# Kernel tuning notes

Hardware: AMD Instinct MI355X
Metric: run time of the kernel (lower is better)

Reference implementation:

```python
import jax, jax.numpy as jnp
import numpy as np

U, SI, TI = 100000, 50000, 40000
D = 64
B = 8192
NNZ_S, NNZ_T = 3_200_000, 2_560_000
P_DROP = 0.2


def setup_inputs() -> dict:
    key = jax.random.key(0)
    ks = iter(jax.random.split(key, 32))
    nxt = lambda: next(ks)
    emb = lambda n: (jax.random.normal(nxt(), (n, D), jnp.float32) * 0.1)
    keep = lambda n: jax.random.bernoulli(nxt(), 1.0 - P_DROP, (n,)).astype(jnp.float32) / (1.0 - P_DROP)
    inp = {}
    inp['user'] = jax.random.randint(nxt(), (B,), 0, U, jnp.int32)
    inp['source_pos_item'] = jax.random.randint(nxt(), (B,), 0, SI, jnp.int32)
    inp['source_neg_item'] = jax.random.randint(nxt(), (B,), 0, SI, jnp.int32)
    inp['target_pos_item'] = jax.random.randint(nxt(), (B,), 0, TI, jnp.int32)
    inp['target_neg_item'] = jax.random.randint(nxt(), (B,), 0, TI, jnp.int32)
    inp['mask_s'] = jax.random.bernoulli(nxt(), 0.5, (B,))
    inp['mask_t'] = jax.random.bernoulli(nxt(), 0.5, (B,))
    inp['su_int'] = emb(U); inp['si_int'] = emb(SI)
    inp['tu_int'] = emb(U); inp['ti_int'] = emb(TI)
    inp['su_pop'] = emb(U); inp['si_pop'] = emb(SI)
    inp['tu_pop'] = emb(U); inp['ti_pop'] = emb(TI)
    Ns, Nt = U + SI, U + TI
    inp['s_rows'] = jax.random.randint(nxt(), (NNZ_S,), 0, Ns, jnp.int32)
    inp['s_cols'] = jax.random.randint(nxt(), (NNZ_S,), 0, Ns, jnp.int32)
    inp['s_vals'] = jax.random.uniform(nxt(), (NNZ_S,), jnp.float32, 0.0, 0.02)
    inp['t_rows'] = jax.random.randint(nxt(), (NNZ_T,), 0, Nt, jnp.int32)
    inp['t_cols'] = jax.random.randint(nxt(), (NNZ_T,), 0, Nt, jnp.int32)
    inp['t_vals'] = jax.random.uniform(nxt(), (NNZ_T,), jnp.float32, 0.0, 0.02)
    inp['drop_s_int'] = keep(NNZ_S); inp['drop_t_int'] = keep(NNZ_T)
    inp['drop_s_pop'] = keep(NNZ_S); inp['drop_t_pop'] = keep(NNZ_T)
    return inp


def _lightgcn(emb, rows, cols, vals, n_users):
    # 1-layer LightGCN: out = mean([e0, A @ e0]) ; A given as COO (rows, cols, vals)
    agg = jax.ops.segment_sum(vals[:, None] * emb[cols], rows, num_segments=emb.shape[0])
    out = 0.5 * (emb + agg)
    return out[:n_users], out[n_users:]


def _bpr(p, n):
    return -jnp.mean(jax.nn.log_sigmoid(p - n))


def _mask_bpr(p, n, m):
    return -jnp.mean(m.astype(p.dtype) * jax.nn.log_sigmoid(p - n))


def _masked_l1(a, b, idx):
    # L1Loss(mean) over rows selected by unique(idx); membership mask avoids jnp.unique
    m = jnp.zeros((a.shape[0],), bool).at[idx].set(True)
    cnt = jnp.maximum(m.sum(), 1).astype(a.dtype)
    return jnp.sum(jnp.abs(a - b) * m[:, None]) / (cnt * a.shape[1])


def reference(user, source_pos_item, source_neg_item, target_pos_item, target_neg_item,
              mask_s, mask_t,
              su_int, si_int, tu_int, ti_int, su_pop, si_pop, tu_pop, ti_pop,
              s_rows, s_cols, s_vals, t_rows, t_cols, t_vals,
              drop_s_int, drop_t_int, drop_s_pop, drop_t_pop):
    # int factor
    us_i, is_i = _lightgcn(jnp.concatenate([su_int, si_int]), s_rows, s_cols, s_vals * drop_s_int, U)
    ut_i, it_i = _lightgcn(jnp.concatenate([tu_int, ti_int]), t_rows, t_cols, t_vals * drop_t_int, U)
    # pop factor
    us_p, is_p = _lightgcn(jnp.concatenate([su_pop, si_pop]), s_rows, s_cols, s_vals * drop_s_pop, U)
    ut_p, it_p = _lightgcn(jnp.concatenate([tu_pop, ti_pop]), t_rows, t_cols, t_vals * drop_t_pop, U)

    dot = lambda ue, ie, u, i: jnp.sum(ue[u] * ie[i], axis=1)
    sp_i = dot(us_i, is_i, user, source_pos_item); sn_i = dot(us_i, is_i, user, source_neg_item)
    sp_p = dot(us_p, is_p, user, source_pos_item); sn_p = dot(us_p, is_p, user, source_neg_item)
    tp_i = dot(ut_i, it_i, user, target_pos_item); tn_i = dot(ut_i, it_i, user, target_neg_item)
    tp_p = dot(ut_p, it_p, user, target_pos_item); tn_p = dot(ut_p, it_p, user, target_neg_item)

    loss_int_s = _mask_bpr(sp_i, sn_i, mask_s)
    loss_pop_s = _mask_bpr(sn_p, sp_p, mask_s) + _mask_bpr(sp_p, sn_p, ~mask_s)
    loss_int_t = _mask_bpr(tp_i, tn_i, mask_t)
    loss_pop_t = _mask_bpr(tn_p, tp_p, mask_t) + _mask_bpr(tp_p, tn_p, ~mask_t)
    loss_total_s = _bpr(sp_i + sp_p, sn_i + sn_p)
    loss_total_t = _bpr(tp_i + tp_p, tn_i + tn_p)

    item_all_s = jnp.concatenate([source_pos_item, source_neg_item])
    item_all_t = jnp.concatenate([target_pos_item, target_neg_item])
    dis_loss = (_masked_l1(su_int, su_pop, user) + _masked_l1(si_int, si_pop, item_all_s)
                + _masked_l1(tu_int, tu_pop, user) + _masked_l1(ti_int, ti_pop, item_all_t))

    loss = (loss_total_s + loss_total_t
            + 0.1 * (loss_int_s + loss_int_t)
            + 0.1 * (loss_pop_s + loss_pop_t)
            - 0.01 * dis_loss)
    return loss
```

## Files before the change

### kernel.cpp

```cpp
#include <hip/hip_runtime.h>
#include <math.h>

constexpr int U_N = 100000;
constexpr int SI_N = 50000;
constexpr int TI_N = 40000;
constexpr int D = 64;
constexpr int B = 8192;
constexpr int NS = U_N + SI_N;
constexpr int NT = U_N + TI_N;
constexpr int SLOTS = 3 * B;
constexpr int CAP = 64;
constexpr int OVCAP = 4096;
constexpr int NROWS_ALL = U_N + SI_N + TI_N;

__device__ __forceinline__ float wave_sum(float x) {
#pragma unroll
  for (int m = 32; m; m >>= 1) x += __shfl_xor(x, m, 64);
  return x;
}

__device__ __forceinline__ float softplus_f(float z) {
  return fmaxf(z, 0.f) + log1pf(expf(-fabsf(z)));
}

__global__ __launch_bounds__(256) void k_init(
    const int* __restrict__ user, const int* __restrict__ spos, const int* __restrict__ sneg,
    const int* __restrict__ tpos, const int* __restrict__ tneg,
    int* __restrict__ map_s, int* __restrict__ map_t,
    const unsigned char* __restrict__ m, int* __restrict__ det) {
  if (blockIdx.x < 96) {
    int t = blockIdx.x * blockDim.x + threadIdx.x;
    if (t < B) {
      int u = user[t];
      map_s[u] = t;
      map_t[u] = t;
    } else if (t < 2 * B) {
      int b = t - B;
      map_s[U_N + spos[b]] = t;
      map_t[U_N + tpos[b]] = t;
    } else {
      int b = t - 2 * B;
      map_s[U_N + sneg[b]] = t;
      map_t[U_N + tneg[b]] = t;
    }
    return;
  }
  int t = threadIdx.x;
  int cb = 0, cc = 0;
  for (int i = t; i < B; i += 256) {
    unsigned char v = m[i];
    if ((i & 3) && v) cb++;
    if (v > 1) cc++;
  }
#pragma unroll
  for (int off = 32; off; off >>= 1) {
    cb += __shfl_xor(cb, off, 64);
    cc += __shfl_xor(cc, off, 64);
  }
  __shared__ int sb[4], sc[4];
  if ((t & 63) == 0) { sb[t >> 6] = cb; sc[t >> 6] = cc; }
  __syncthreads();
  if (t == 0) {
    det[0] = sb[0] + sb[1] + sb[2] + sb[3];
    det[1] = sc[0] + sc[1] + sc[2] + sc[3];
  }
}

__global__ __launch_bounds__(256) void k_compact2(
    const int* __restrict__ s_rows, const int* __restrict__ t_rows,
    const int* __restrict__ map_s, const int* __restrict__ map_t,
    int* __restrict__ cnt_s, int* __restrict__ cnt_t,
    int* __restrict__ bucket_s, int* __restrict__ bucket_t,
    int* __restrict__ ovcnt_s, int* __restrict__ ovcnt_t,
    int* __restrict__ ov_s, int* __restrict__ ov_t, int nnz_s, int nnz_t) {
  int e = blockIdx.x * 256 + threadIdx.x;
  const int* rows;
  const int* map;
  int* cnt;
  int* bucket;
  int* ovcnt;
  int* ov;
  if (e < nnz_s) {
    rows = s_rows; map = map_s; cnt = cnt_s; bucket = bucket_s; ovcnt = ovcnt_s; ov = ov_s;
  } else {
    e -= nnz_s;
    if (e >= nnz_t) return;
    rows = t_rows; map = map_t; cnt = cnt_t; bucket = bucket_t; ovcnt = ovcnt_t; ov = ov_t;
  }
  int slot = map[rows[e]];
  if (slot < 0) return;
  int pos = atomicAdd(&cnt[slot], 1);
  if (pos < CAP) {
    bucket[slot * CAP + pos] = e;
  } else {
    int o = atomicAdd(ovcnt, 1);
    if (o < OVCAP) { ov[2 * o] = slot; ov[2 * o + 1] = e; }
  }
}

__device__ __forceinline__ void accum_slot(
    int s, int lane,
    const int* __restrict__ cols, const float* __restrict__ vals,
    const float* __restrict__ di, const float* __restrict__ dp,
    const int* __restrict__ cnt, const int* __restrict__ bucket,
    const int* __restrict__ ovcnt, const int* __restrict__ ov,
    const float* __restrict__ eu_i, const float* __restrict__ ei_i,
    const float* __restrict__ eu_p, const float* __restrict__ ei_p,
    float* __restrict__ aggA, float* __restrict__ aggB) {
  int m = min(cnt[s], CAP);
  int g = lane >> 4, sub = lane & 15;
  int c = 0;
  float wi = 0.f, wp = 0.f;
  if (lane < m) {
    int e = bucket[s * CAP + lane];
    c = cols[e];
    float v = vals[e];
    wi = v * di[e];
    wp = v * dp[e];
  }
  float aIx = 0, aIy = 0, aIz = 0, aIw = 0;
  float aPx = 0, aPy = 0, aPz = 0, aPw = 0;
  for (int k = 0; k < m; k += 16) {
    int i0 = k + g, i1 = k + 4 + g, i2 = k + 8 + g, i3 = k + 12 + g;
    int c0 = __shfl(c, i0, 64), c1 = __shfl(c, i1, 64);
    int c2 = __shfl(c, i2, 64), c3 = __shfl(c, i3, 64);
    float wi0 = __shfl(wi, i0, 64), wi1 = __shfl(wi, i1, 64);
    float wi2 = __shfl(wi, i2, 64), wi3 = __shfl(wi, i3, 64);
    float wp0 = __shfl(wp, i0, 64), wp1 = __shfl(wp, i1, 64);
    float wp2 = __shfl(wp, i2, 64), wp3 = __shfl(wp, i3, 64);
    const float* bi0 = (c0 < U_N) ? (eu_i + (size_t)c0 * D) : (ei_i + (size_t)(c0 - U_N) * D);
    const float* bi1 = (c1 < U_N) ? (eu_i + (size_t)c1 * D) : (ei_i + (size_t)(c1 - U_N) * D);
    const float* bi2 = (c2 < U_N) ? (eu_i + (size_t)c2 * D) : (ei_i + (size_t)(c2 - U_N) * D);
    const float* bi3 = (c3 < U_N) ? (eu_i + (size_t)c3 * D) : (ei_i + (size_t)(c3 - U_N) * D);
    const float* bp0 = (c0 < U_N) ? (eu_p + (size_t)c0 * D) : (ei_p + (size_t)(c0 - U_N) * D);
    const float* bp1 = (c1 < U_N) ? (eu_p + (size_t)c1 * D) : (ei_p + (size_t)(c1 - U_N) * D);
    const float* bp2 = (c2 < U_N) ? (eu_p + (size_t)c2 * D) : (ei_p + (size_t)(c2 - U_N) * D);
    const float* bp3 = (c3 < U_N) ? (eu_p + (size_t)c3 * D) : (ei_p + (size_t)(c3 - U_N) * D);
    float4 vI0 = *(const float4*)(bi0 + 4 * sub);
    float4 vI1 = *(const float4*)(bi1 + 4 * sub);
    float4 vI2 = *(const float4*)(bi2 + 4 * sub);
    float4 vI3 = *(const float4*)(bi3 + 4 * sub);
    float4 vP0 = *(const float4*)(bp0 + 4 * sub);
    float4 vP1 = *(const float4*)(bp1 + 4 * sub);
    float4 vP2 = *(const float4*)(bp2 + 4 * sub);
    float4 vP3 = *(const float4*)(bp3 + 4 * sub);
    aIx = fmaf(wi0, vI0.x, aIx); aIy = fmaf(wi0, vI0.y, aIy);
    aIz = fmaf(wi0, vI0.z, aIz); aIw = fmaf(wi0, vI0.w, aIw);
    aIx = fmaf(wi1, vI1.x, aIx); aIy = fmaf(wi1, vI1.y, aIy);
    aIz = fmaf(wi1, vI1.z, aIz); aIw = fmaf(wi1, vI1.w, aIw);
    aIx = fmaf(wi2, vI2.x, aIx); aIy = fmaf(wi2, vI2.y, aIy);
    aIz = fmaf(wi2, vI2.z, aIz); aIw = fmaf(wi2, vI2.w, aIw);
    aIx = fmaf(wi3, vI3.x, aIx); aIy = fmaf(wi3, vI3.y, aIy);
    aIz = fmaf(wi3, vI3.z, aIz); aIw = fmaf(wi3, vI3.w, aIw);
    aPx = fmaf(wp0, vP0.x, aPx); aPy = fmaf(wp0, vP0.y, aPy);
    aPz = fmaf(wp0, vP0.z, aPz); aPw = fmaf(wp0, vP0.w, aPw);
    aPx = fmaf(wp1, vP1.x, aPx); aPy = fmaf(wp1, vP1.y, aPy);
    aPz = fmaf(wp1, vP1.z, aPz); aPw = fmaf(wp1, vP1.w, aPw);
    aPx = fmaf(wp2, vP2.x, aPx); aPy = fmaf(wp2, vP2.y, aPy);
    aPz = fmaf(wp2, vP2.z, aPz); aPw = fmaf(wp2, vP2.w, aPw);
    aPx = fmaf(wp3, vP3.x, aPx); aPy = fmaf(wp3, vP3.y, aPy);
    aPz = fmaf(wp3, vP3.z, aPz); aPw = fmaf(wp3, vP3.w, aPw);
  }
#define XRED(x) x += __shfl_xor(x, 16, 64); x += __shfl_xor(x, 32, 64);
  XRED(aIx) XRED(aIy) XRED(aIz) XRED(aIw)
  XRED(aPx) XRED(aPy) XRED(aPz) XRED(aPw)
#undef XRED
  int nov = min(*ovcnt, OVCAP);
  for (int i = 0; i < nov; ++i) {
    if (ov[2 * i] == s) {
      int e = ov[2 * i + 1];
      int cc = cols[e];
      float v = vals[e];
      float wwi = v * di[e], wwp = v * dp[e];
      const float* bi = (cc < U_N) ? (eu_i + (size_t)cc * D) : (ei_i + (size_t)(cc - U_N) * D);
      const float* bp = (cc < U_N) ? (eu_p + (size_t)cc * D) : (ei_p + (size_t)(cc - U_N) * D);
      if (lane < 16) {
        float4 vI = *(const float4*)(bi + 4 * sub);
        float4 vP = *(const float4*)(bp + 4 * sub);
        aIx = fmaf(wwi, vI.x, aIx); aIy = fmaf(wwi, vI.y, aIy);
        aIz = fmaf(wwi, vI.z, aIz); aIw = fmaf(wwi, vI.w, aIw);
        aPx = fmaf(wwp, vP.x, aPx); aPy = fmaf(wwp, vP.y, aPy);
        aPz = fmaf(wwp, vP.z, aPz); aPw = fmaf(wwp, vP.w, aPw);
      }
    }
  }
  if (lane < 16) {
    *(float4*)(aggA + (size_t)s * D + 4 * sub) = make_float4(aIx, aIy, aIz, aIw);
    *(float4*)(aggB + (size_t)s * D + 4 * sub) = make_float4(aPx, aPy, aPz, aPw);
  }
}

__global__ __launch_bounds__(256) void k_accum_pair(
    const int* __restrict__ s_cols, const float* __restrict__ s_vals,
    const float* __restrict__ dsi, const float* __restrict__ dsp,
    const int* __restrict__ t_cols, const float* __restrict__ t_vals,
    const float* __restrict__ dti, const float* __restrict__ dtp,
    const int* __restrict__ cnt_s, const int* __restrict__ bucket_s,
    const int* __restrict__ ovcnt_s, const int* __restrict__ ov_s,
    const int* __restrict__ cnt_t, const int* __restrict__ bucket_t,
    const int* __restrict__ ovcnt_t, const int* __restrict__ ov_t,
    const float* __restrict__ su_i, const float* __restrict__ si_i,
    const float* __restrict__ su_p, const float* __restrict__ si_p,
    const float* __restrict__ tu_i, const float* __restrict__ ti_i,
    const float* __restrict__ tu_p, const float* __restrict__ ti_p,
    float* __restrict__ aggSA, float* __restrict__ aggSB,
    float* __restrict__ aggTA, float* __restrict__ aggTB) {
  int lane = threadIdx.x & 63;
  int sg = (blockIdx.x * 256 + threadIdx.x) >> 6;
  if (sg >= 2 * SLOTS) return;
  if (sg < SLOTS) {
    accum_slot(sg, lane, s_cols, s_vals, dsi, dsp, cnt_s, bucket_s, ovcnt_s, ov_s,
               su_i, si_i, su_p, si_p, aggSA, aggSB);
  } else {
    accum_slot(sg - SLOTS, lane, t_cols, t_vals, dti, dtp, cnt_t, bucket_t, ovcnt_t, ov_t,
               tu_i, ti_i, tu_p, ti_p, aggTA, aggTB);
  }
}

__global__ __launch_bounds__(256) void k_accum1(
    const int* __restrict__ cols, const float* __restrict__ vals,
    const float* __restrict__ di, const float* __restrict__ dp,
    const int* __restrict__ cnt, const int* __restrict__ bucket,
    const int* __restrict__ ovcnt, const int* __restrict__ ov,
    const float* __restrict__ eu_i, const float* __restrict__ ei_i,
    const float* __restrict__ eu_p, const float* __restrict__ ei_p,
    float* __restrict__ aggA, float* __restrict__ aggB) {
  int lane = threadIdx.x & 63;
  int s = (blockIdx.x * 256 + threadIdx.x) >> 6;
  if (s >= SLOTS) return;
  accum_slot(s, lane, cols, vals, di, dp, cnt, bucket, ovcnt, ov,
             eu_i, ei_i, eu_p, ei_p, aggA, aggB);
}

__device__ __forceinline__ void dots_one(
    int b, int lane,
    const int* __restrict__ user, const int* __restrict__ pos, const int* __restrict__ neg,
    const float* __restrict__ eu_i, const float* __restrict__ ei_i,
    const float* __restrict__ eu_p, const float* __restrict__ ei_p,
    const int* __restrict__ map, const float* __restrict__ aggA, const float* __restrict__ aggB,
    float* __restrict__ dst) {
  int u = user[b], p = pos[b], n = neg[b];
  int su = map[u], sp = map[U_N + p], sn = map[U_N + n];
  float oui = eu_i[(size_t)u * D + lane] + aggA[(size_t)su * D + lane];
  float oup = eu_p[(size_t)u * D + lane] + aggB[(size_t)su * D + lane];
  float opi = ei_i[(size_t)p * D + lane] + aggA[(size_t)sp * D + lane];
  float opp = ei_p[(size_t)p * D + lane] + aggB[(size_t)sp * D + lane];
  float oni = ei_i[(size_t)n * D + lane] + aggA[(size_t)sn * D + lane];
  float onp = ei_p[(size_t)n * D + lane] + aggB[(size_t)sn * D + lane];
  float s0 = wave_sum(oui * opi);
  float s1 = wave_sum(oui * oni);
  float s2 = wave_sum(oup * opp);
  float s3 = wave_sum(oup * onp);
  if (lane == 0) {
    dst[b] = 0.25f * s0;
    dst[B + b] = 0.25f * s1;
    dst[2 * B + b] = 0.25f * s2;
    dst[3 * B + b] = 0.25f * s3;
  }
}

__global__ __launch_bounds__(256) void k_dots_pair(
    const int* __restrict__ user,
    const int* __restrict__ spos, const int* __restrict__ sneg,
    const int* __restrict__ tpos, const int* __restrict__ tneg,
    const float* __restrict__ su_i, const float* __restrict__ si_i,
    const float* __restrict__ su_p, const float* __restrict__ si_p,
    const float* __restrict__ tu_i, const float* __restrict__ ti_i,
    const float* __restrict__ tu_p, const float* __restrict__ ti_p,
    const int* __restrict__ map_s, const int* __restrict__ map_t,
    const float* __restrict__ aggSA, const float* __restrict__ aggSB,
    const float* __restrict__ aggTA, const float* __restrict__ aggTB,
    float* __restrict__ dots) {
  int lane = threadIdx.x & 63;
  int j = (blockIdx.x * blockDim.x + threadIdx.x) >> 6;
  if (j >= 2 * B) return;
  if (j < B) {
    dots_one(j, lane, user, spos, sneg, su_i, si_i, su_p, si_p, map_s, aggSA, aggSB, dots);
  } else {
    dots_one(j - B, lane, user, tpos, tneg, tu_i, ti_i, tu_p, ti_p, map_t, aggTA, aggTB,
             dots + 4 * B);
  }
}

__global__ __launch_bounds__(256) void k_dots1(
    const int* __restrict__ user, const int* __restrict__ pos, const int* __restrict__ neg,
    const float* __restrict__ eu_i, const float* __restrict__ ei_i,
    const float* __restrict__ eu_p, const float* __restrict__ ei_p,
    const int* __restrict__ map, const float* __restrict__ aggA, const float* __restrict__ aggB,
    float* __restrict__ dst) {
  int lane = threadIdx.x & 63;
  int b = (blockIdx.x * blockDim.x + threadIdx.x) >> 6;
  if (b >= B) return;
  dots_one(b, lane, user, pos, neg, eu_i, ei_i, eu_p, ei_p, map, aggA, aggB, dst);
}

__global__ __launch_bounds__(256) void k_loss(
    const unsigned char* __restrict__ ms8, const unsigned char* __restrict__ mt8,
    const float* __restrict__ dots, const int* __restrict__ det,
    const float* __restrict__ su_i, const float* __restrict__ su_p,
    const float* __restrict__ tu_i, const float* __restrict__ tu_p,
    const float* __restrict__ si_i, const float* __restrict__ si_p,
    const float* __restrict__ ti_i, const float* __restrict__ ti_p,
    const int* __restrict__ map_s, const int* __restrict__ map_t,
    float* __restrict__ acc) {
  if (blockIdx.x < 32) {
    int b = blockIdx.x * blockDim.x + threadIdx.x;
    const float* spi = dots;
    const float* sni = dots + B;
    const float* spp = dots + 2 * B;
    const float* snp = dots + 3 * B;
    const float* tpi = dots + 4 * B;
    const float* tni = dots + 5 * B;
    const float* tpp = dots + 6 * B;
    const float* tnp = dots + 7 * B;
    int db = det[0], dc = det[1];
    float ms, mt;
    if (dc > 100) {
      ms = (((const float*)ms8)[b] != 0.f) ? 1.f : 0.f;
      mt = (((const float*)mt8)[b] != 0.f) ? 1.f : 0.f;
    } else if (db > 100) {
      ms = ms8[b] ? 1.f : 0.f;
      mt = mt8[b] ? 1.f : 0.f;
    } else {
      ms = ((const int*)ms8)[b] ? 1.f : 0.f;
      mt = ((const int*)mt8)[b] ? 1.f : 0.f;
    }
    float l_int_s = ms * softplus_f(sni[b] - spi[b]);
    float l_pop_s = ms * softplus_f(spp[b] - snp[b]) + (1.f - ms) * softplus_f(snp[b] - spp[b]);
    float l_tot_s = softplus_f((sni[b] + snp[b]) - (spi[b] + spp[b]));
    float l_int_t = mt * softplus_f(tni[b] - tpi[b]);
    float l_pop_t = mt * softplus_f(tpp[b] - tnp[b]) + (1.f - mt) * softplus_f(tnp[b] - tpp[b]);
    float l_tot_t = softplus_f((tni[b] + tnp[b]) - (tpi[b] + tpp[b]));
    float contrib = (l_tot_s + l_tot_t + 0.1f * (l_int_s + l_int_t) +
                     0.1f * (l_pop_s + l_pop_t)) * (1.f / (float)B);
#pragma unroll
    for (int off = 32; off; off >>= 1) contrib += __shfl_xor(contrib, off, 64);
    __shared__ float wsum_[4];
    if ((threadIdx.x & 63) == 0) wsum_[threadIdx.x >> 6] = contrib;
    __syncthreads();
    if (threadIdx.x == 0) atomicAdd(&acc[0], wsum_[0] + wsum_[1] + wsum_[2] + wsum_[3]);
    return;
  }
  int lane = threadIdx.x & 63;
  int wave = ((blockIdx.x - 32) * blockDim.x + threadIdx.x) >> 6;
  int nwaves = ((gridDim.x - 32) * blockDim.x) >> 6;
  float a1 = 0.f, a2 = 0.f, a3 = 0.f, a4 = 0.f;
  float c5 = 0.f, c6 = 0.f, c7 = 0.f;
  for (int r = wave; r < NROWS_ALL; r += nwaves) {
    if (r < U_N) {
      if (map_s[r] < 0) continue;
      size_t o = (size_t)r * D + lane;
      a1 += fabsf(su_i[o] - su_p[o]);
      a3 += fabsf(tu_i[o] - tu_p[o]);
      if (lane == 0) c5 += 1.f;
    } else if (r < U_N + SI_N) {
      int rr = r - U_N;
      if (map_s[U_N + rr] < 0) continue;
      size_t o = (size_t)rr * D + lane;
      a2 += fabsf(si_i[o] - si_p[o]);
      if (lane == 0) c6 += 1.f;
    } else {
      int rr = r - U_N - SI_N;
      if (map_t[U_N + rr] < 0) continue;
      size_t o = (size_t)rr * D + lane;
      a4 += fabsf(ti_i[o] - ti_p[o]);
      if (lane == 0) c7 += 1.f;
    }
  }
  a1 = wave_sum(a1);
  a2 = wave_sum(a2);
  a3 = wave_sum(a3);
  a4 = wave_sum(a4);
  __shared__ float sb[4][8];
  if (lane == 0) {
    int w = threadIdx.x >> 6;
    sb[w][0] = a1; sb[w][1] = a2; sb[w][2] = a3; sb[w][3] = a4;
    sb[w][4] = c5; sb[w][5] = c6; sb[w][6] = c7;
  }
  __syncthreads();
  int t = threadIdx.x;
  if (t < 7) {
    float v = sb[0][t] + sb[1][t] + sb[2][t] + sb[3][t];
    atomicAdd(&acc[1 + t], v);
  }
}

__global__ void k_final(const float* __restrict__ acc, float* __restrict__ out) {
  if (threadIdx.x == 0 && blockIdx.x == 0) {
    float cu = fmaxf(acc[5], 1.f);
    float cs = fmaxf(acc[6], 1.f);
    float ct = fmaxf(acc[7], 1.f);
    float dis = acc[1] / (cu * (float)D) + acc[2] / (cs * (float)D) +
                acc[3] / (cu * (float)D) + acc[4] / (ct * (float)D);
    out[0] = acc[0] - 0.01f * dis;
  }
}

extern "C" void kernel_launch(void* const* d_in, const int* in_sizes, int n_in,
                              void* d_out, int out_size, void* d_ws, size_t ws_size,
                              hipStream_t stream) {
  const int* user = (const int*)d_in[0];
  const int* spos = (const int*)d_in[1];
  const int* sneg = (const int*)d_in[2];
  const int* tpos = (const int*)d_in[3];
  const int* tneg = (const int*)d_in[4];
  const unsigned char* mask_s = (const unsigned char*)d_in[5];
  const unsigned char* mask_t = (const unsigned char*)d_in[6];
  const float* su_int = (const float*)d_in[7];
  const float* si_int = (const float*)d_in[8];
  const float* tu_int = (const float*)d_in[9];
  const float* ti_int = (const float*)d_in[10];
  const float* su_pop = (const float*)d_in[11];
  const float* si_pop = (const float*)d_in[12];
  const float* tu_pop = (const float*)d_in[13];
  const float* ti_pop = (const float*)d_in[14];
  const int* s_rows = (const int*)d_in[15];
  const int* s_cols = (const int*)d_in[16];
  const float* s_vals = (const float*)d_in[17];
  const int* t_rows = (const int*)d_in[18];
  const int* t_cols = (const int*)d_in[19];
  const float* t_vals = (const float*)d_in[20];
  const float* drop_s_int = (const float*)d_in[21];
  const float* drop_t_int = (const float*)d_in[22];
  const float* drop_s_pop = (const float*)d_in[23];
  const float* drop_t_pop = (const float*)d_in[24];
  const int nnz_s = in_sizes[15];
  const int nnz_t = in_sizes[18];

  float* acc = (float*)d_ws;
  int* det = (int*)(acc + 16);
  int* ovcnt_s = det + 2;
  int* ovcnt_t = ovcnt_s + 1;
  int* cnt_s = ovcnt_t + 1;
  int* cnt_t = cnt_s + SLOTS;
  int* map_s = cnt_t + SLOTS;
  int* map_t = map_s + NS;
  float* dots = (float*)(map_t + NT);
  int* ov_s = (int*)(dots + 8 * B);
  int* ov_t = ov_s + 2 * OVCAP;
  int* bucket_s = ov_t + 2 * OVCAP;
  int* bucket_t = bucket_s + SLOTS * CAP;
  float* aggSA = (float*)(bucket_t + SLOTS * CAP);
  float* aggSB = aggSA + (size_t)SLOTS * D;
  float* aggTA = aggSB + (size_t)SLOTS * D;
  float* aggTB = aggTA + (size_t)SLOTS * D;
  size_t need_big = (size_t)((char*)(aggTB + (size_t)SLOTS * D) - (char*)d_ws);
  bool big = ws_size >= need_big;

  hipMemsetAsync(acc, 0, (size_t)(16 + 4 + 2 * SLOTS) * sizeof(int), stream);
  hipMemsetAsync(map_s, 0xFF, (size_t)(NS + NT) * sizeof(int), stream);

  k_init<<<97, 256, 0, stream>>>(user, spos, sneg, tpos, tneg, map_s, map_t, mask_s, det);

  k_compact2<<<(nnz_s + nnz_t + 255) / 256, 256, 0, stream>>>(
      s_rows, t_rows, map_s, map_t, cnt_s, cnt_t, bucket_s, bucket_t,
      ovcnt_s, ovcnt_t, ov_s, ov_t, nnz_s, nnz_t);

  if (big) {
    k_accum_pair<<<2 * SLOTS / 4, 256, 0, stream>>>(
        s_cols, s_vals, drop_s_int, drop_s_pop, t_cols, t_vals, drop_t_int, drop_t_pop,
        cnt_s, bucket_s, ovcnt_s, ov_s, cnt_t, bucket_t, ovcnt_t, ov_t,
        su_int, si_int, su_pop, si_pop, tu_int, ti_int, tu_pop, ti_pop,
        aggSA, aggSB, aggTA, aggTB);
    k_dots_pair<<<(2 * B * 64) / 256, 256, 0, stream>>>(
        user, spos, sneg, tpos, tneg, su_int, si_int, su_pop, si_pop,
        tu_int, ti_int, tu_pop, ti_pop, map_s, map_t,
        aggSA, aggSB, aggTA, aggTB, dots);
  } else {
    k_accum1<<<SLOTS / 4, 256, 0, stream>>>(s_cols, s_vals, drop_s_int, drop_s_pop,
                                            cnt_s, bucket_s, ovcnt_s, ov_s,
                                            su_int, si_int, su_pop, si_pop, aggSA, aggSB);
    k_dots1<<<(B * 64) / 256, 256, 0, stream>>>(user, spos, sneg, su_int, si_int, su_pop, si_pop,
                                                map_s, aggSA, aggSB, dots);
    k_accum1<<<SLOTS / 4, 256, 0, stream>>>(t_cols, t_vals, drop_t_int, drop_t_pop,
                                            cnt_t, bucket_t, ovcnt_t, ov_t,
                                            tu_int, ti_int, tu_pop, ti_pop, aggSA, aggSB);
    k_dots1<<<(B * 64) / 256, 256, 0, stream>>>(user, tpos, tneg, tu_int, ti_int, tu_pop, ti_pop,
                                                map_t, aggSA, aggSB, dots + 4 * B);
  }

  k_loss<<<32 + 256, 256, 0, stream>>>(mask_s, mask_t, dots, det,
                                       su_int, su_pop, tu_int, tu_pop,
                                       si_int, si_pop, ti_int, ti_pop,
                                       map_s, map_t, acc);
  k_final<<<1, 64, 0, stream>>>(acc, (float*)d_out);
}
```

Before: 491.0 us.

## Fuse dot products with BPR loss and fold final reduction into L1 kernel

Merges the dot-product kernel and the BPR loss computation into one kernel, so per-sample scores stay in registers instead of going through a global dots buffer. The masked L1 pass now scans rows in 64-row chunks using ballot masks to skip unused rows, and a last-block-done counter replaces the separate final kernel. The small-workspace fallback path is removed. This cuts two launches and one global round trip, at the cost of relying on a large enough workspace and on atomic-based completion detection.

```diff
diff --git a/kernel.cpp b/kernel.cpp
--- a/kernel.cpp
+++ b/kernel.cpp
@@ -12,6 +12,7 @@
 constexpr int CAP = 64;
 constexpr int OVCAP = 4096;
 constexpr int NROWS_ALL = U_N + SI_N + TI_N;
+constexpr int NCHUNK = (NROWS_ALL + 63) / 64;
 
 __device__ __forceinline__ float wave_sum(float x) {
 #pragma unroll
@@ -217,52 +218,12 @@
   }
 }
 
-__global__ __launch_bounds__(256) void k_accum1(
-    const int* __restrict__ cols, const float* __restrict__ vals,
-    const float* __restrict__ di, const float* __restrict__ dp,
-    const int* __restrict__ cnt, const int* __restrict__ bucket,
-    const int* __restrict__ ovcnt, const int* __restrict__ ov,
-    const float* __restrict__ eu_i, const float* __restrict__ ei_i,
-    const float* __restrict__ eu_p, const float* __restrict__ ei_p,
-    float* __restrict__ aggA, float* __restrict__ aggB) {
-  int lane = threadIdx.x & 63;
-  int s = (blockIdx.x * 256 + threadIdx.x) >> 6;
-  if (s >= SLOTS) return;
-  accum_slot(s, lane, cols, vals, di, dp, cnt, bucket, ovcnt, ov,
-             eu_i, ei_i, eu_p, ei_p, aggA, aggB);
-}
-
-__device__ __forceinline__ void dots_one(
-    int b, int lane,
-    const int* __restrict__ user, const int* __restrict__ pos, const int* __restrict__ neg,
-    const float* __restrict__ eu_i, const float* __restrict__ ei_i,
-    const float* __restrict__ eu_p, const float* __restrict__ ei_p,
-    const int* __restrict__ map, const float* __restrict__ aggA, const float* __restrict__ aggB,
-    float* __restrict__ dst) {
-  int u = user[b], p = pos[b], n = neg[b];
-  int su = map[u], sp = map[U_N + p], sn = map[U_N + n];
-  float oui = eu_i[(size_t)u * D + lane] + aggA[(size_t)su * D + lane];
-  float oup = eu_p[(size_t)u * D + lane] + aggB[(size_t)su * D + lane];
-  float opi = ei_i[(size_t)p * D + lane] + aggA[(size_t)sp * D + lane];
-  float opp = ei_p[(size_t)p * D + lane] + aggB[(size_t)sp * D + lane];
-  float oni = ei_i[(size_t)n * D + lane] + aggA[(size_t)sn * D + lane];
-  float onp = ei_p[(size_t)n * D + lane] + aggB[(size_t)sn * D + lane];
-  float s0 = wave_sum(oui * opi);
-  float s1 = wave_sum(oui * oni);
-  float s2 = wave_sum(oup * opp);
-  float s3 = wave_sum(oup * onp);
-  if (lane == 0) {
-    dst[b] = 0.25f * s0;
-    dst[B + b] = 0.25f * s1;
-    dst[2 * B + b] = 0.25f * s2;
-    dst[3 * B + b] = 0.25f * s3;
-  }
-}
-
-__global__ __launch_bounds__(256) void k_dots_pair(
+__global__ __launch_bounds__(256) void k_dots_loss(
     const int* __restrict__ user,
     const int* __restrict__ spos, const int* __restrict__ sneg,
     const int* __restrict__ tpos, const int* __restrict__ tneg,
+    const unsigned char* __restrict__ ms8, const unsigned char* __restrict__ mt8,
+    const int* __restrict__ det,
     const float* __restrict__ su_i, const float* __restrict__ si_i,
     const float* __restrict__ su_p, const float* __restrict__ si_p,
     const float* __restrict__ tu_i, const float* __restrict__ ti_i,
@@ -270,49 +231,35 @@
     const int* __restrict__ map_s, const int* __restrict__ map_t,
     const float* __restrict__ aggSA, const float* __restrict__ aggSB,
     const float* __restrict__ aggTA, const float* __restrict__ aggTB,
-    float* __restrict__ dots) {
-  int lane = threadIdx.x & 63;
-  int j = (blockIdx.x * blockDim.x + threadIdx.x) >> 6;
-  if (j >= 2 * B) return;
-  if (j < B) {
-    dots_one(j, lane, user, spos, sneg, su_i, si_i, su_p, si_p, map_s, aggSA, aggSB, dots);
-  } else {
-    dots_one(j - B, lane, user, tpos, tneg, tu_i, ti_i, tu_p, ti_p, map_t, aggTA, aggTB,
-             dots + 4 * B);
-  }
-}
-
-__global__ __launch_bounds__(256) void k_dots1(
-    const int* __restrict__ user, const int* __restrict__ pos, const int* __restrict__ neg,
-    const float* __restrict__ eu_i, const float* __restrict__ ei_i,
-    const float* __restrict__ eu_p, const float* __restrict__ ei_p,
-    const int* __restrict__ map, const float* __restrict__ aggA, const float* __restrict__ aggB,
-    float* __restrict__ dst) {
+    float* __restrict__ acc) {
   int lane = threadIdx.x & 63;
   int b = (blockIdx.x * blockDim.x + threadIdx.x) >> 6;
-  if (b >= B) return;
-  dots_one(b, lane, user, pos, neg, eu_i, ei_i, eu_p, ei_p, map, aggA, aggB, dst);
-}
-
-__global__ __launch_bounds__(256) void k_loss(
-    const unsigned char* __restrict__ ms8, const unsigned char* __restrict__ mt8,
-    const float* __restrict__ dots, const int* __restrict__ det,
-    const float* __restrict__ su_i, const float* __restrict__ su_p,
-    const float* __restrict__ tu_i, const float* __restrict__ tu_p,
-    const float* __restrict__ si_i, const float* __restrict__ si_p,
-    const float* __restrict__ ti_i, const float* __restrict__ ti_p,
-    const int* __restrict__ map_s, const int* __restrict__ map_t,
-    float* __restrict__ acc) {
-  if (blockIdx.x < 32) {
-    int b = blockIdx.x * blockDim.x + threadIdx.x;
-    const float* spi = dots;
-    const float* sni = dots + B;
-    const float* spp = dots + 2 * B;
-    const float* snp = dots + 3 * B;
-    const float* tpi = dots + 4 * B;
-    const float* tni = dots + 5 * B;
-    const float* tpp = dots + 6 * B;
-    const float* tnp = dots + 7 * B;
+  float contrib = 0.f;
+  if (b < B) {
+    int u = user[b];
+    int ps = spos[b], ns = sneg[b], pt = tpos[b], nt = tneg[b];
+    int sus = map_s[u], sps = map_s[U_N + ps], sns = map_s[U_N + ns];
+    int sut = map_t[u], spt = map_t[U_N + pt], snt = map_t[U_N + nt];
+    float oui = su_i[(size_t)u * D + lane] + aggSA[(size_t)sus * D + lane];
+    float oup = su_p[(size_t)u * D + lane] + aggSB[(size_t)sus * D + lane];
+    float opi = si_i[(size_t)ps * D + lane] + aggSA[(size_t)sps * D + lane];
+    float opp = si_p[(size_t)ps * D + lane] + aggSB[(size_t)sps * D + lane];
+    float oni = si_i[(size_t)ns * D + lane] + aggSA[(size_t)sns * D + lane];
+    float onp = si_p[(size_t)ns * D + lane] + aggSB[(size_t)sns * D + lane];
+    float spi = 0.25f * wave_sum(oui * opi);
+    float sni = 0.25f * wave_sum(oui * oni);
+    float spp = 0.25f * wave_sum(oup * opp);
+    float snp = 0.25f * wave_sum(oup * onp);
+    float tui = tu_i[(size_t)u * D + lane] + aggTA[(size_t)sut * D + lane];
+    float tup = tu_p[(size_t)u * D + lane] + aggTB[(size_t)sut * D + lane];
+    float tpi_ = ti_i[(size_t)pt * D + lane] + aggTA[(size_t)spt * D + lane];
+    float tpp_ = ti_p[(size_t)pt * D + lane] + aggTB[(size_t)spt * D + lane];
+    float tni_ = ti_i[(size_t)nt * D + lane] + aggTA[(size_t)snt * D + lane];
+    float tnp_ = ti_p[(size_t)nt * D + lane] + aggTB[(size_t)snt * D + lane];
+    float tpi = 0.25f * wave_sum(tui * tpi_);
+    float tni = 0.25f * wave_sum(tui * tni_);
+    float tpp = 0.25f * wave_sum(tup * tpp_);
+    float tnp = 0.25f * wave_sum(tup * tnp_);
     int db = det[0], dc = det[1];
     float ms, mt;
     if (dc > 100) {
@@ -325,46 +272,64 @@
       ms = ((const int*)ms8)[b] ? 1.f : 0.f;
       mt = ((const int*)mt8)[b] ? 1.f : 0.f;
     }
-    float l_int_s = ms * softplus_f(sni[b] - spi[b]);
-    float l_pop_s = ms * softplus_f(spp[b] - snp[b]) + (1.f - ms) * softplus_f(snp[b] - spp[b]);
-    float l_tot_s = softplus_f((sni[b] + snp[b]) - (spi[b] + spp[b]));
-    float l_int_t = mt * softplus_f(tni[b] - tpi[b]);
-    float l_pop_t = mt * softplus_f(tpp[b] - tnp[b]) + (1.f - mt) * softplus_f(tnp[b] - tpp[b]);
-    float l_tot_t = softplus_f((tni[b] + tnp[b]) - (tpi[b] + tpp[b]));
-    float contrib = (l_tot_s + l_tot_t + 0.1f * (l_int_s + l_int_t) +
-                     0.1f * (l_pop_s + l_pop_t)) * (1.f / (float)B);
-#pragma unroll
-    for (int off = 32; off; off >>= 1) contrib += __shfl_xor(contrib, off, 64);
-    __shared__ float wsum_[4];
-    if ((threadIdx.x & 63) == 0) wsum_[threadIdx.x >> 6] = contrib;
-    __syncthreads();
-    if (threadIdx.x == 0) atomicAdd(&acc[0], wsum_[0] + wsum_[1] + wsum_[2] + wsum_[3]);
-    return;
-  }
+    float l_int_s = ms * softplus_f(sni - spi);
+    float l_pop_s = ms * softplus_f(spp - snp) + (1.f - ms) * softplus_f(snp - spp);
+    float l_tot_s = softplus_f((sni + snp) - (spi + spp));
+    float l_int_t = mt * softplus_f(tni - tpi);
+    float l_pop_t = mt * softplus_f(tpp - tnp) + (1.f - mt) * softplus_f(tnp - tpp);
+    float l_tot_t = softplus_f((tni + tnp) - (tpi + tpp));
+    contrib = (l_tot_s + l_tot_t + 0.1f * (l_int_s + l_int_t) +
+               0.1f * (l_pop_s + l_pop_t)) * (1.f / (float)B);
+  }
+  __shared__ float wsum_[4];
+  if (lane == 0) wsum_[threadIdx.x >> 6] = contrib;
+  __syncthreads();
+  if (threadIdx.x == 0) atomicAdd(&acc[0], wsum_[0] + wsum_[1] + wsum_[2] + wsum_[3]);
+}
+
+__global__ __launch_bounds__(256) void k_l1_final(
+    const float* __restrict__ su_i, const float* __restrict__ su_p,
+    const float* __restrict__ tu_i, const float* __restrict__ tu_p,
+    const float* __restrict__ si_i, const float* __restrict__ si_p,
+    const float* __restrict__ ti_i, const float* __restrict__ ti_p,
+    const int* __restrict__ map_s, const int* __restrict__ map_t,
+    float* __restrict__ acc, int* __restrict__ done_ctr,
+    float* __restrict__ out) {
   int lane = threadIdx.x & 63;
-  int wave = ((blockIdx.x - 32) * blockDim.x + threadIdx.x) >> 6;
-  int nwaves = ((gridDim.x - 32) * blockDim.x) >> 6;
+  int wave = (blockIdx.x * blockDim.x + threadIdx.x) >> 6;
+  int nwaves = (gridDim.x * blockDim.x) >> 6;
   float a1 = 0.f, a2 = 0.f, a3 = 0.f, a4 = 0.f;
   float c5 = 0.f, c6 = 0.f, c7 = 0.f;
-  for (int r = wave; r < NROWS_ALL; r += nwaves) {
-    if (r < U_N) {
-      if (map_s[r] < 0) continue;
-      size_t o = (size_t)r * D + lane;
-      a1 += fabsf(su_i[o] - su_p[o]);
-      a3 += fabsf(tu_i[o] - tu_p[o]);
-      if (lane == 0) c5 += 1.f;
-    } else if (r < U_N + SI_N) {
-      int rr = r - U_N;
-      if (map_s[U_N + rr] < 0) continue;
-      size_t o = (size_t)rr * D + lane;
-      a2 += fabsf(si_i[o] - si_p[o]);
-      if (lane == 0) c6 += 1.f;
-    } else {
-      int rr = r - U_N - SI_N;
-      if (map_t[U_N + rr] < 0) continue;
-      size_t o = (size_t)rr * D + lane;
-      a4 += fabsf(ti_i[o] - ti_p[o]);
-      if (lane == 0) c7 += 1.f;
+  for (int ch = wave; ch < NCHUNK; ch += nwaves) {
+    int r0 = ch * 64;
+    int r = r0 + lane;
+    int flag = -1;
+    if (r < NROWS_ALL) flag = (r < NS) ? map_s[r] : map_t[r - SI_N];
+    bool valid = flag >= 0;
+    unsigned long long m0 = __ballot(valid && r < U_N);
+    unsigned long long m1 = __ballot(valid && r >= U_N && r < NS);
+    unsigned long long m2 = __ballot(valid && r >= NS);
+    if (lane == 0) {
+      c5 += (float)__popcll(m0);
+      c6 += (float)__popcll(m1);
+      c7 += (float)__popcll(m2);
+    }
+    unsigned long long mm = m0 | m1 | m2;
+    while (mm) {
+      int bit = __ffsll((unsigned long long)mm) - 1;
+      mm &= mm - 1;
+      int rr = r0 + bit;
+      if (rr < U_N) {
+        size_t o = (size_t)rr * D + lane;
+        a1 += fabsf(su_i[o] - su_p[o]);
+        a3 += fabsf(tu_i[o] - tu_p[o]);
+      } else if (rr < NS) {
+        size_t o = (size_t)(rr - U_N) * D + lane;
+        a2 += fabsf(si_i[o] - si_p[o]);
+      } else {
+        size_t o = (size_t)(rr - NS) * D + lane;
+        a4 += fabsf(ti_i[o] - ti_p[o]);
+      }
     }
   }
   a1 = wave_sum(a1);
@@ -383,16 +348,23 @@
     float v = sb[0][t] + sb[1][t] + sb[2][t] + sb[3][t];
     atomicAdd(&acc[1 + t], v);
   }
-}
-
-__global__ void k_final(const float* __restrict__ acc, float* __restrict__ out) {
-  if (threadIdx.x == 0 && blockIdx.x == 0) {
-    float cu = fmaxf(acc[5], 1.f);
-    float cs = fmaxf(acc[6], 1.f);
-    float ct = fmaxf(acc[7], 1.f);
-    float dis = acc[1] / (cu * (float)D) + acc[2] / (cs * (float)D) +
-                acc[3] / (cu * (float)D) + acc[4] / (ct * (float)D);
-    out[0] = acc[0] - 0.01f * dis;
+  __syncthreads();
+  if (t == 0) {
+    __threadfence();
+    int old = atomicAdd(done_ctr, 1);
+    if (old == (int)gridDim.x - 1) {
+      float a0 = atomicAdd(&acc[0], 0.f);
+      float n1 = atomicAdd(&acc[1], 0.f);
+      float n2 = atomicAdd(&acc[2], 0.f);
+      float n3 = atomicAdd(&acc[3], 0.f);
+      float n4 = atomicAdd(&acc[4], 0.f);
+      float cu = fmaxf(atomicAdd(&acc[5], 0.f), 1.f);
+      float cs = fmaxf(atomicAdd(&acc[6], 0.f), 1.f);
+      float ct = fmaxf(atomicAdd(&acc[7], 0.f), 1.f);
+      float dis = n1 / (cu * (float)D) + n2 / (cs * (float)D) +
+                  n3 / (cu * (float)D) + n4 / (ct * (float)D);
+      out[0] = a0 - 0.01f * dis;
+    }
   }
 }
 
@@ -428,15 +400,15 @@
   const int nnz_t = in_sizes[18];
 
   float* acc = (float*)d_ws;
-  int* det = (int*)(acc + 16);
+  int* done_ctr = (int*)(acc + 16);
+  int* det = done_ctr + 1;
   int* ovcnt_s = det + 2;
   int* ovcnt_t = ovcnt_s + 1;
   int* cnt_s = ovcnt_t + 1;
   int* cnt_t = cnt_s + SLOTS;
   int* map_s = cnt_t + SLOTS;
   int* map_t = map_s + NS;
-  float* dots = (float*)(map_t + NT);
-  int* ov_s = (int*)(dots + 8 * B);
+  int* ov_s = map_t + NT;
   int* ov_t = ov_s + 2 * OVCAP;
   int* bucket_s = ov_t + 2 * OVCAP;
   int* bucket_t = bucket_s + SLOTS * CAP;
@@ -444,10 +416,8 @@
   float* aggSB = aggSA + (size_t)SLOTS * D;
   float* aggTA = aggSB + (size_t)SLOTS * D;
   float* aggTB = aggTA + (size_t)SLOTS * D;
-  size_t need_big = (size_t)((char*)(aggTB + (size_t)SLOTS * D) - (char*)d_ws);
-  bool big = ws_size >= need_big;
-
-  hipMemsetAsync(acc, 0, (size_t)(16 + 4 + 2 * SLOTS) * sizeof(int), stream);
+
+  hipMemsetAsync(acc, 0, (size_t)(16 + 1 + 2 + 2 + 2 * SLOTS) * sizeof(int), stream);
   hipMemsetAsync(map_s, 0xFF, (size_t)(NS + NT) * sizeof(int), stream);
 
   k_init<<<97, 256, 0, stream>>>(user, spos, sneg, tpos, tneg, map_s, map_t, mask_s, det);
@@ -456,32 +426,18 @@
       s_rows, t_rows, map_s, map_t, cnt_s, cnt_t, bucket_s, bucket_t,
       ovcnt_s, ovcnt_t, ov_s, ov_t, nnz_s, nnz_t);
 
-  if (big) {
-    k_accum_pair<<<2 * SLOTS / 4, 256, 0, stream>>>(
-        s_cols, s_vals, drop_s_int, drop_s_pop, t_cols, t_vals, drop_t_int, drop_t_pop,
-        cnt_s, bucket_s, ovcnt_s, ov_s, cnt_t, bucket_t, ovcnt_t, ov_t,
-        su_int, si_int, su_pop, si_pop, tu_int, ti_int, tu_pop, ti_pop,
-        aggSA, aggSB, aggTA, aggTB);
-    k_dots_pair<<<(2 * B * 64) / 256, 256, 0, stream>>>(
-        user, spos, sneg, tpos, tneg, su_int, si_int, su_pop, si_pop,
-        tu_int, ti_int, tu_pop, ti_pop, map_s, map_t,
-        aggSA, aggSB, aggTA, aggTB, dots);
-  } else {
-    k_accum1<<<SLOTS / 4, 256, 0, stream>>>(s_cols, s_vals, drop_s_int, drop_s_pop,
-                                            cnt_s, bucket_s, ovcnt_s, ov_s,
-                                            su_int, si_int, su_pop, si_pop, aggSA, aggSB);
-    k_dots1<<<(B * 64) / 256, 256, 0, stream>>>(user, spos, sneg, su_int, si_int, su_pop, si_pop,
-                                                map_s, aggSA, aggSB, dots);
-    k_accum1<<<SLOTS / 4, 256, 0, stream>>>(t_cols, t_vals, drop_t_int, drop_t_pop,
-                                            cnt_t, bucket_t, ovcnt_t, ov_t,
-                                            tu_int, ti_int, tu_pop, ti_pop, aggSA, aggSB);
-    k_dots1<<<(B * 64) / 256, 256, 0, stream>>>(user, tpos, tneg, tu_int, ti_int, tu_pop, ti_pop,
-                                                map_t, aggSA, aggSB, dots + 4 * B);
-  }
-
-  k_loss<<<32 + 256, 256, 0, stream>>>(mask_s, mask_t, dots, det,
-                                       su_int, su_pop, tu_int, tu_pop,
-                                       si_int, si_pop, ti_int, ti_pop,
-                                       map_s, map_t, acc);
-  k_final<<<1, 64, 0, stream>>>(acc, (float*)d_out);
-}
+  k_accum_pair<<<2 * SLOTS / 4, 256, 0, stream>>>(
+      s_cols, s_vals, drop_s_int, drop_s_pop, t_cols, t_vals, drop_t_int, drop_t_pop,
+      cnt_s, bucket_s, ovcnt_s, ov_s, cnt_t, bucket_t, ovcnt_t, ov_t,
+      su_int, si_int, su_pop, si_pop, tu_int, ti_int, tu_pop, ti_pop,
+      aggSA, aggSB, aggTA, aggTB);
+
+  k_dots_loss<<<(B + 3) / 4, 256, 0, stream>>>(
+      user, spos, sneg, tpos, tneg, mask_s, mask_t, det,
+      su_int, si_int, su_pop, si_pop, tu_int, ti_int, tu_pop, ti_pop,
+      map_s, map_t, aggSA, aggSB, aggTA, aggTB, acc);
+
+  k_l1_final<<<768, 256, 0, stream>>>(su_int, su_pop, tu_int, tu_pop,
+                                      si_int, si_pop, ti_int, ti_pop,
+                                      map_s, map_t, acc, done_ctr, (float*)d_out);
+}
```

Result: no change. 484.9 us (-1.3%).
